# Performance work log

Measured on AMD Instinct MI355X. Metric: run time of the kernel, lower is better.

The kernel has to match this reference:

```python
import jax, jax.numpy as jnp
import numpy as np


def _gcn_conv(h_in, W, b, src, dst, deg_isqrt, n_nodes):
    # PyG GCNConv: out = D^{-1/2} (A + I) D^{-1/2} (h_in @ W) + b
    # src/dst already include self-loops; deg_isqrt precomputed on self-looped graph.
    h = h_in @ W                                   # [N, hid]
    norm = deg_isqrt[src] * deg_isqrt[dst]         # [E+N]
    msg = h[src] * norm[:, None]                   # gather + scale
    agg = jax.ops.segment_sum(msg, dst, num_segments=n_nodes)  # scatter-add
    return agg + b


def setup_inputs() -> dict:
    key = jax.random.key(0)
    ks = jax.random.split(key, 8)
    N, E, P, IN, HID = 100000, 1600000, 400000, 128, 64
    x = jax.random.normal(ks[0], (N, IN), dtype=jnp.float32)
    edge_index = jax.random.randint(ks[1], (2, E), 0, N, dtype=jnp.int64)
    batch = jax.random.randint(ks[2], (N,), 0, 64, dtype=jnp.int64)
    pairs = jax.random.randint(ks[3], (P, 2), 0, N, dtype=jnp.int64)
    s1 = 1.0 / np.sqrt(IN)
    s2 = 1.0 / np.sqrt(HID)
    W1 = jax.random.normal(ks[4], (IN, HID), dtype=jnp.float32) * s1
    b1 = jnp.zeros((HID,), dtype=jnp.float32)
    W2 = jax.random.normal(ks[5], (HID, HID), dtype=jnp.float32) * s2
    b2 = jnp.zeros((HID,), dtype=jnp.float32)
    Wh = jax.random.normal(ks[6], (2 * HID, 1), dtype=jnp.float32) * s2
    bh = jnp.zeros((1,), dtype=jnp.float32)
    return {"x": x, "edge_index": edge_index, "batch": batch, "pairs": pairs,
            "W1": W1, "b1": b1, "W2": W2, "b2": b2, "Wh": Wh, "bh": bh}


def reference(x, edge_index, batch, pairs, W1, b1, W2, b2, Wh, bh):
    n_nodes = x.shape[0]
    loops = jnp.arange(n_nodes, dtype=edge_index.dtype)
    src = jnp.concatenate([edge_index[0], loops])
    dst = jnp.concatenate([edge_index[1], loops])
    # degree on self-looped graph (counted at dst, PyG convention)
    deg = jax.ops.segment_sum(jnp.ones_like(dst, dtype=x.dtype), dst,
                              num_segments=n_nodes)
    deg_isqrt = jnp.where(deg > 0, jax.lax.rsqrt(deg), 0.0)

    h = jax.nn.relu(_gcn_conv(x, W1, b1, src, dst, deg_isqrt, n_nodes))
    h = jax.nn.relu(_gcn_conv(h, W2, b2, src, dst, deg_isqrt, n_nodes))

    emb = jnp.concatenate([h[pairs[:, 0]], h[pairs[:, 1]]], axis=-1)  # [P, 2*hid]
    out = (emb @ Wh + bh)[:, 0]                                        # [P]
    return out
```

## Files before the change

### kernel.cpp

```cpp
#include <hip/hip_runtime.h>

#define THREADS 256
#define BNODES 256
#define PACK_SHIFT 20
#define TILE 8192

__device__ __forceinline__ unsigned short f2bf(float f) {
    unsigned u = __float_as_uint(f);
    unsigned r = (u + 0x7fff + ((u >> 16) & 1)) >> 16;
    return (unsigned short)r;
}
__device__ __forceinline__ float bf2f_lo(unsigned v) { return __uint_as_float(v << 16); }
__device__ __forceinline__ float bf2f_hi(unsigned v) { return __uint_as_float(v & 0xffff0000u); }


__global__ __launch_bounds__(256) void count_buckets(const int* __restrict__ dst,
                                                     int* __restrict__ subcnt,
                                                     int NB, int E) {
    __shared__ int h[1024];
    int t = threadIdx.x;
    for (int i = t; i < NB; i += 256) h[i] = 0;
    __syncthreads();
    int e0 = blockIdx.x * TILE;
    int e1 = min(e0 + TILE, E);
    for (int e = e0 + t; e < e1; e += 256)
        atomicAdd(&h[dst[e] >> 8], 1);
    __syncthreads();
    for (int i = t; i < NB; i += 256)
        if (h[i] > 0) atomicAdd(&subcnt[i], h[i]);
}

__global__ void scan_small_kernel(const int* __restrict__ cnt, int* __restrict__ ptr,
                                  int nb, int total) {
    __shared__ int sh[1024];
    int t = threadIdx.x;
    int v = (t < nb) ? cnt[t] : 0;
    sh[t] = v;
    __syncthreads();
    for (int off = 1; off < 1024; off <<= 1) {
        int add = (t >= off) ? sh[t - off] : 0;
        __syncthreads();
        sh[t] += add;
        __syncthreads();
    }
    if (t < nb) ptr[t] = sh[t] - v;
    if (t == 0) ptr[nb] = total;
}

__global__ __launch_bounds__(256) void block_scatter(const int* __restrict__ src,
                                                     const int* __restrict__ dst,
                                                     const int* __restrict__ subptr,
                                                     int* __restrict__ subcur,
                                                     int* __restrict__ ebuf,
                                                     int NB, int E) {
    __shared__ int h[1024];
    __shared__ int bb[1024];
    int t = threadIdx.x;
    for (int i = t; i < NB; i += 256) h[i] = 0;
    __syncthreads();
    int e0 = blockIdx.x * TILE;
    int e1 = min(e0 + TILE, E);
    for (int e = e0 + t; e < e1; e += 256)
        atomicAdd(&h[dst[e] >> 8], 1);
    __syncthreads();
    for (int i = t; i < NB; i += 256) {
        int c = h[i];
        bb[i] = (c > 0) ? (subptr[i] + atomicAdd(&subcur[i], c)) : 0;
        h[i] = 0;
    }
    __syncthreads();
    for (int e = e0 + t; e < e1; e += 256) {
        int d = dst[e];
        int b = d >> 8;
        int pos = bb[b] + atomicAdd(&h[b], 1);
        ebuf[pos] = src[e] | ((d & (BNODES - 1)) << PACK_SHIFT);
    }
}

__global__ __launch_bounds__(256) void bin_fill_kernel(const int* __restrict__ ebuf,
                                                       const int* __restrict__ subptr,
                                                       int* __restrict__ rowptr,
                                                       float* __restrict__ dis,
                                                       int* __restrict__ srcs,
                                                       int NB, int N, int E) {
    __shared__ int cntL[BNODES];
    __shared__ int rb[BNODES];
    int b = blockIdx.x;
    int t = threadIdx.x;
    int base = b * BNODES;
    int s0 = subptr[b], s1 = subptr[b + 1];
    cntL[t] = 0;
    __syncthreads();
    for (int i = s0 + t; i < s1; i += 256)
        atomicAdd(&cntL[((unsigned)ebuf[i]) >> PACK_SHIFT], 1);
    __syncthreads();
    int myc = cntL[t];
    if (base + t < N) dis[base + t] = rsqrtf((float)myc + 1.0f);
    rb[t] = myc;
    __syncthreads();
    #pragma unroll
    for (int off = 1; off < 256; off <<= 1) {
        int add = (t >= off) ? rb[t - off] : 0;
        __syncthreads();
        rb[t] += add;
        __syncthreads();
    }
    int excl = rb[t] - myc;
    rb[t] = s0 + excl;
    if (base + t < N) rowptr[base + t] = s0 + excl;
    if (b == NB - 1 && t == 0) rowptr[N] = E;
    cntL[t] = 0;
    __syncthreads();
    const int mask = (1 << PACK_SHIFT) - 1;
    for (int i = s0 + t; i < s1; i += 256) {
        int w = ebuf[i];
        int local = ((unsigned)w) >> PACK_SHIFT;
        int pos = rb[local] + atomicAdd(&cntL[local], 1);
        srcs[pos] = w & mask;
    }
}

template<int K, bool SCALE, typename YT>
__global__ __launch_bounds__(256, 4) void gemm_tiled(const float* __restrict__ X,
                                                     const float* __restrict__ W,
                                                     const float* __restrict__ dis,
                                                     YT* __restrict__ Y, int M) {
    __shared__ float Ws[32 * 64];
    __shared__ float Xs[32 * 68];
    const int t = threadIdx.x;

    const int r0 = blockIdx.x * 64;
    const int wave = t >> 6;
    const int lane = t & 63;
    const int tr = lane & 15;
    const int tc = (lane >> 4) + wave * 4;

    float acc[4][4] = {};

    #pragma unroll 1
    for (int kc = 0; kc < K; kc += 32) {
        __syncthreads();
        #pragma unroll
        for (int it = 0; it < 2; ++it) {
            int i = it * 256 + t;
            ((float4*)Ws)[i] = ((const float4*)(W + (size_t)kc * 64))[i];
        }
        #pragma unroll
        for (int it = 0; it < 2; ++it) {
            int i = it * 256 + t;
            int row = i & 63;
            int kq = i >> 6;
            int gr = r0 + row;
            if (gr >= M) gr = M - 1;
            float4 v = *(const float4*)(X + (size_t)gr * K + kc + kq * 4);
            Xs[(kq * 4 + 0) * 68 + row] = v.x;
            Xs[(kq * 4 + 1) * 68 + row] = v.y;
            Xs[(kq * 4 + 2) * 68 + row] = v.z;
            Xs[(kq * 4 + 3) * 68 + row] = v.w;
        }
        __syncthreads();
        #pragma unroll
        for (int kk = 0; kk < 32; ++kk) {
            float4 xv = *(const float4*)(Xs + kk * 68 + tr * 4);
            float4 wv = *(const float4*)(Ws + kk * 64 + tc * 4);
            acc[0][0] = fmaf(xv.x, wv.x, acc[0][0]);
            acc[0][1] = fmaf(xv.x, wv.y, acc[0][1]);
            acc[0][2] = fmaf(xv.x, wv.z, acc[0][2]);
            acc[0][3] = fmaf(xv.x, wv.w, acc[0][3]);
            acc[1][0] = fmaf(xv.y, wv.x, acc[1][0]);
            acc[1][1] = fmaf(xv.y, wv.y, acc[1][1]);
            acc[1][2] = fmaf(xv.y, wv.z, acc[1][2]);
            acc[1][3] = fmaf(xv.y, wv.w, acc[1][3]);
            acc[2][0] = fmaf(xv.z, wv.x, acc[2][0]);
            acc[2][1] = fmaf(xv.z, wv.y, acc[2][1]);
            acc[2][2] = fmaf(xv.z, wv.z, acc[2][2]);
            acc[2][3] = fmaf(xv.z, wv.w, acc[2][3]);
            acc[3][0] = fmaf(xv.w, wv.x, acc[3][0]);
            acc[3][1] = fmaf(xv.w, wv.y, acc[3][1]);
            acc[3][2] = fmaf(xv.w, wv.z, acc[3][2]);
            acc[3][3] = fmaf(xv.w, wv.w, acc[3][3]);
        }
    }

    #pragma unroll
    for (int i = 0; i < 4; ++i) {
        int row = r0 + tr * 4 + i;
        if (row < M) {
            float s = SCALE ? dis[row] : 1.0f;
            if constexpr (sizeof(YT) == 2) {
                ushort4 st;
                st.x = f2bf(acc[i][0] * s);
                st.y = f2bf(acc[i][1] * s);
                st.z = f2bf(acc[i][2] * s);
                st.w = f2bf(acc[i][3] * s);
                *(ushort4*)((unsigned short*)Y + (size_t)row * 64 + tc * 4) = st;
            } else {
                float4 st = make_float4(acc[i][0] * s, acc[i][1] * s,
                                        acc[i][2] * s, acc[i][3] * s);
                *(float4*)((float*)Y + (size_t)row * 64 + tc * 4) = st;
            }
        }
    }
}

template<bool HEAD>
__global__ __launch_bounds__(256) void pull2_kernel(const unsigned* __restrict__ hpre2,
                                                    const int* __restrict__ rowptr,
                                                    const int* __restrict__ srcs,
                                                    const float* __restrict__ dis,
                                                    const float* __restrict__ b,
                                                    const float* __restrict__ Wh,
                                                    float* __restrict__ out,
                                                    float2* __restrict__ s01, int N) {
    int tid = threadIdx.x;
    int wave = tid >> 6;
    int lane = tid & 63;
    int l = lane & 31;
    int node = blockIdx.x * 8 + wave * 2 + (lane >> 5);
    bool valid = node < N;
    int nc = valid ? node : N - 1;
    int i = rowptr[nc];
    int end = valid ? rowptr[nc + 1] : i;

    unsigned sv = hpre2[(size_t)nc * 32 + l];
    float accx = bf2f_lo(sv), accy = bf2f_hi(sv);

    while (__any(i < end)) {
        #pragma unroll
        for (int k = 0; k < 8; ++k) {
            int idx = i + k;
            bool m = idx < end;
            int s = srcs[m ? idx : 0];
            unsigned v = hpre2[(size_t)s * 32 + l];
            accx += m ? bf2f_lo(v) : 0.f;
            accy += m ? bf2f_hi(v) : 0.f;
        }
        i += 8;
    }

    float d = dis[nc];
    float2 bb = ((const float2*)b)[l];
    float ox = accx * d + bb.x;
    float oy = accy * d + bb.y;
    ox = ox > 0.f ? ox : 0.f;
    oy = oy > 0.f ? oy : 0.f;

    if (HEAD) {
        float2 w0 = ((const float2*)Wh)[l];
        float2 w1 = ((const float2*)(Wh + 64))[l];
        float p0 = ox * w0.x + oy * w0.y;
        float p1 = ox * w1.x + oy * w1.y;
        #pragma unroll
        for (int off = 16; off > 0; off >>= 1) {
            p0 += __shfl_down(p0, off, 32);
            p1 += __shfl_down(p1, off, 32);
        }
        if (valid && l == 0) s01[node] = make_float2(p0, p1);
    } else {
        if (valid) *(float2*)(out + (size_t)node * 64 + 2 * l) = make_float2(ox, oy);
    }
}

__global__ void pair_kernel(const float2* __restrict__ s01, const int* __restrict__ pairs,
                            const float* __restrict__ bh, float* __restrict__ out, int P) {
    int p = blockIdx.x * blockDim.x + threadIdx.x;
    if (p < P) {
        int p0 = pairs[2 * (size_t)p];
        int p1 = pairs[2 * (size_t)p + 1];
        out[p] = s01[p0].x + s01[p1].y + bh[0];
    }
}

__global__ void degf_kernel(const int* __restrict__ dst, float* __restrict__ deg, int E) {
    int e = blockIdx.x * blockDim.x + threadIdx.x;
    if (e < E) atomicAdd(&deg[dst[e]], 1.0f);
}
__global__ void rsqrtf_kernel(float* deg, int N) {
    int i = blockIdx.x * blockDim.x + threadIdx.x;
    if (i < N) deg[i] = rsqrtf(deg[i] + 1.0f);
}
__global__ void scatter_kernel(const float* __restrict__ h, const int* __restrict__ src,
                               const int* __restrict__ dst, const float* __restrict__ dis,
                               float* __restrict__ agg, int E, int N) {
    long long idx = (long long)blockIdx.x * blockDim.x + threadIdx.x;
    int e = (int)(idx >> 6);
    int f = (int)(idx & 63);
    if (e >= E + N) return;
    int s, d;
    if (e < E) { s = src[e]; d = dst[e]; } else { s = e - E; d = s; }
    float norm = dis[s] * dis[d];
    atomicAdd(&agg[(size_t)d * 64 + f], h[(size_t)s * 64 + f] * norm);
}
__global__ void bias_relu_kernel(float* __restrict__ buf, const float* __restrict__ b,
                                 long long total) {
    long long i = (long long)blockIdx.x * blockDim.x + threadIdx.x;
    if (i < total) {
        float v = buf[i] + b[(int)(i & 63)];
        buf[i] = v > 0.f ? v : 0.f;
    }
}
__global__ void head_kernel(const float* __restrict__ h, const int* __restrict__ pairs,
                            const float* __restrict__ Wh, const float* __restrict__ bh,
                            float* __restrict__ out, int P) {
    long long idx = (long long)blockIdx.x * blockDim.x + threadIdx.x;
    int p = (int)(idx >> 6);
    int lane = threadIdx.x & 63;
    if (p >= P) return;
    int p0 = pairs[2 * (size_t)p];
    int p1 = pairs[2 * (size_t)p + 1];
    float v = h[(size_t)p0 * 64 + lane] * Wh[lane]
            + h[(size_t)p1 * 64 + lane] * Wh[64 + lane];
    #pragma unroll
    for (int off = 32; off > 0; off >>= 1) v += __shfl_down(v, off);
    if (lane == 0) out[p] = v + bh[0];
}

extern "C" void kernel_launch(void* const* d_in, const int* in_sizes, int n_in,
                              void* d_out, int out_size, void* d_ws, size_t ws_size,
                              hipStream_t stream) {
    const float* x     = (const float*)d_in[0];
    const int*   ei    = (const int*)d_in[1];
    const int*   pairs = (const int*)d_in[3];
    const float* W1    = (const float*)d_in[4];
    const float* b1    = (const float*)d_in[5];
    const float* W2    = (const float*)d_in[6];
    const float* b2    = (const float*)d_in[7];
    const float* Wh    = (const float*)d_in[8];
    const float* bh    = (const float*)d_in[9];

    const int N = in_sizes[0] / 128;
    const int E = in_sizes[1] / 2;
    const int P = in_sizes[3] / 2;
    const int* srcArr = ei;
    const int* dstArr = ei + E;

    const size_t feat_total = (size_t)N * 64;
    const int NB = (N + BNODES - 1) / BNODES;
    const int tileBlocks = (E + TILE - 1) / TILE;
    const int gemm_blocks = (N + 63) / 64;
    const int pull_blocks = (N + 7) / 8;

    auto align512 = [](size_t v) { return (v + 511) & ~(size_t)511; };

    char* ws = (char*)d_ws;
    size_t off = 0;
    float*  dis    = (float*) (ws + off); off += align512((size_t)N * 4);
    int*    rowptr = (int*)   (ws + off); off += align512(((size_t)N + 1) * 4);
    int*    subcnt = (int*)   (ws + off); off += align512((size_t)NB * 4);
    int*    subcur = (int*)   (ws + off); off += align512((size_t)NB * 4);
    int*    subptr = (int*)   (ws + off); off += align512(((size_t)NB + 1) * 4);
    float2* s01    = (float2*)(ws + off); off += align512((size_t)N * 8);
    int*    srcs   = (int*)   (ws + off); off += align512((size_t)E * 4);
    size_t bufA_bytes = align512((size_t)E * 4 > feat_total * 2 ? (size_t)E * 4
                                                                : feat_total * 2);
    unsigned short* bufA = (unsigned short*)(ws + off); off += bufA_bytes;
    float*  bufB   = (float*) (ws + off); off += align512(feat_total * 4);
    int*    ebuf   = (int*)bufA;
    const bool csr_ok = (off <= ws_size) && (NB <= 1024) && (N <= (1 << PACK_SHIFT));

    if (csr_ok) {
        hipMemsetAsync(subcnt, 0, (size_t)NB * 4, stream);
        hipMemsetAsync(subcur, 0, (size_t)NB * 4, stream);
        count_buckets<<<tileBlocks, 256, 0, stream>>>(dstArr, subcnt, NB, E);
        scan_small_kernel<<<1, 1024, 0, stream>>>(subcnt, subptr, NB, E);
        block_scatter<<<tileBlocks, 256, 0, stream>>>(srcArr, dstArr, subptr, subcur,
                                                      ebuf, NB, E);
        bin_fill_kernel<<<NB, 256, 0, stream>>>(ebuf, subptr, rowptr, dis, srcs, NB, N, E);

        gemm_tiled<128, true, unsigned short><<<gemm_blocks, THREADS, 0, stream>>>(
            x, W1, dis, bufA, N);
        pull2_kernel<false><<<pull_blocks, THREADS, 0, stream>>>(
            (const unsigned*)bufA, rowptr, srcs, dis, b1, nullptr, bufB, nullptr, N);

        gemm_tiled<64, true, unsigned short><<<gemm_blocks, THREADS, 0, stream>>>(
            bufB, W2, dis, bufA, N);
        pull2_kernel<true><<<pull_blocks, THREADS, 0, stream>>>(
            (const unsigned*)bufA, rowptr, srcs, dis, b2, Wh, nullptr, s01, N);

        pair_kernel<<<(P + THREADS - 1) / THREADS, THREADS, 0, stream>>>(
            s01, pairs, bh, (float*)d_out, P);
    } else {
        size_t o2 = 0;
        float* deg  = (float*)(ws + o2); o2 += align512((size_t)N * 4);
        float* bA   = (float*)(ws + o2); o2 += align512(feat_total * 4);
        float* bB   = (float*)(ws + o2);
        const size_t edge_threads = (size_t)(E + N) * 64;
        const int eblocks = (E + THREADS - 1) / THREADS;

        hipMemsetAsync(deg, 0, (size_t)N * 4, stream);
        degf_kernel<<<eblocks, THREADS, 0, stream>>>(dstArr, deg, E);
        rsqrtf_kernel<<<(N + THREADS - 1) / THREADS, THREADS, 0, stream>>>(deg, N);

        gemm_tiled<128, false, float><<<gemm_blocks, THREADS, 0, stream>>>(x, W1, deg, bA, N);
        hipMemsetAsync(bB, 0, feat_total * 4, stream);
        scatter_kernel<<<(unsigned)((edge_threads + THREADS - 1) / THREADS), THREADS, 0, stream>>>(
            bA, srcArr, dstArr, deg, bB, E, N);
        bias_relu_kernel<<<(unsigned)((feat_total + THREADS - 1) / THREADS), THREADS, 0, stream>>>(
            bB, b1, (long long)feat_total);

        gemm_tiled<64, false, float><<<gemm_blocks, THREADS, 0, stream>>>(bB, W2, deg, bA, N);
        hipMemsetAsync(bB, 0, feat_total * 4, stream);
        scatter_kernel<<<(unsigned)((edge_threads + THREADS - 1) / THREADS), THREADS, 0, stream>>>(
            bA, srcArr, dstArr, deg, bB, E, N);
        bias_relu_kernel<<<(unsigned)((feat_total + THREADS - 1) / THREADS), THREADS, 0, stream>>>(
            bB, b2, (long long)feat_total);

        head_kernel<<<(unsigned)(((size_t)P * 64 + THREADS - 1) / THREADS), THREADS, 0, stream>>>(
            bB, pairs, Wh, bh, (float*)d_out, P);
    }
}
```

Measured before the change: 198.8 us.

## Split pull gather across two edge streams, fuse memsets, shrink bucket tile

The pull kernel now has each 32-lane half-wave handle two edges at a time: 16 lanes per edge each load a uint2 (four bf16 features), and the two partial sums are combined with a shuffle. This doubles the number of independent row gathers in flight and widens each load. The two memsets become a single zeroing kernel launch, and the bucket tile size shrinks so the count and scatter passes get more blocks. Extra shuffles and partly idle lanes on the final store are the cost, and smaller tiles add more global atomics on the bucket counters.

```diff
diff --git a/kernel.cpp b/kernel.cpp
--- a/kernel.cpp
+++ b/kernel.cpp
@@ -3,7 +3,7 @@
 #define THREADS 256
 #define BNODES 256
 #define PACK_SHIFT 20
-#define TILE 8192
+#define TILE 2048
 
 __device__ __forceinline__ unsigned short f2bf(float f) {
     unsigned u = __float_as_uint(f);
@@ -13,6 +13,10 @@
 __device__ __forceinline__ float bf2f_lo(unsigned v) { return __uint_as_float(v << 16); }
 __device__ __forceinline__ float bf2f_hi(unsigned v) { return __uint_as_float(v & 0xffff0000u); }
 
+
+__global__ void zero2_kernel(int* __restrict__ a, int* __restrict__ b, int n) {
+    for (int i = threadIdx.x; i < n; i += 1024) { a[i] = 0; b[i] = 0; }
+}
 
 __global__ __launch_bounds__(256) void count_buckets(const int* __restrict__ dst,
                                                      int* __restrict__ subcnt,
@@ -213,51 +217,69 @@
                                                     float* __restrict__ out,
                                                     float2* __restrict__ s01, int N) {
     int tid = threadIdx.x;
-    int wave = tid >> 6;
     int lane = tid & 63;
-    int l = lane & 31;
-    int node = blockIdx.x * 8 + wave * 2 + (lane >> 5);
+    int half = lane >> 5;
+    int sub = lane & 31;
+    int eo = sub >> 4;
+    int l = sub & 15;
+    int node = blockIdx.x * 8 + (tid >> 6) * 2 + half;
     bool valid = node < N;
     int nc = valid ? node : N - 1;
-    int i = rowptr[nc];
-    int end = valid ? rowptr[nc + 1] : i;
-
-    unsigned sv = hpre2[(size_t)nc * 32 + l];
-    float accx = bf2f_lo(sv), accy = bf2f_hi(sv);
-
+    int i0 = rowptr[nc];
+    int end = valid ? rowptr[nc + 1] : i0;
+
+    uint2 sv = *(const uint2*)(hpre2 + (size_t)nc * 32 + 2 * l);
+    float a0 = eo ? 0.f : bf2f_lo(sv.x);
+    float a1 = eo ? 0.f : bf2f_hi(sv.x);
+    float a2 = eo ? 0.f : bf2f_lo(sv.y);
+    float a3 = eo ? 0.f : bf2f_hi(sv.y);
+
+    int i = i0 + eo;
     while (__any(i < end)) {
         #pragma unroll
-        for (int k = 0; k < 8; ++k) {
-            int idx = i + k;
+        for (int k = 0; k < 4; ++k) {
+            int idx = i + 2 * k;
             bool m = idx < end;
             int s = srcs[m ? idx : 0];
-            unsigned v = hpre2[(size_t)s * 32 + l];
-            accx += m ? bf2f_lo(v) : 0.f;
-            accy += m ? bf2f_hi(v) : 0.f;
+            uint2 v = *(const uint2*)(hpre2 + (size_t)s * 32 + 2 * l);
+            a0 += m ? bf2f_lo(v.x) : 0.f;
+            a1 += m ? bf2f_hi(v.x) : 0.f;
+            a2 += m ? bf2f_lo(v.y) : 0.f;
+            a3 += m ? bf2f_hi(v.y) : 0.f;
         }
         i += 8;
     }
 
+    a0 += __shfl_down(a0, 16, 32);
+    a1 += __shfl_down(a1, 16, 32);
+    a2 += __shfl_down(a2, 16, 32);
+    a3 += __shfl_down(a3, 16, 32);
+
     float d = dis[nc];
-    float2 bb = ((const float2*)b)[l];
-    float ox = accx * d + bb.x;
-    float oy = accy * d + bb.y;
-    ox = ox > 0.f ? ox : 0.f;
-    oy = oy > 0.f ? oy : 0.f;
+    float4 bb = ((const float4*)b)[l];
+    float o0 = fmaf(a0, d, bb.x);
+    float o1 = fmaf(a1, d, bb.y);
+    float o2 = fmaf(a2, d, bb.z);
+    float o3 = fmaf(a3, d, bb.w);
+    o0 = o0 > 0.f ? o0 : 0.f;
+    o1 = o1 > 0.f ? o1 : 0.f;
+    o2 = o2 > 0.f ? o2 : 0.f;
+    o3 = o3 > 0.f ? o3 : 0.f;
 
     if (HEAD) {
-        float2 w0 = ((const float2*)Wh)[l];
-        float2 w1 = ((const float2*)(Wh + 64))[l];
-        float p0 = ox * w0.x + oy * w0.y;
-        float p1 = ox * w1.x + oy * w1.y;
+        float4 w0 = ((const float4*)Wh)[l];
+        float4 w1 = ((const float4*)(Wh + 64))[l];
+        float p0 = o0 * w0.x + o1 * w0.y + o2 * w0.z + o3 * w0.w;
+        float p1 = o0 * w1.x + o1 * w1.y + o2 * w1.z + o3 * w1.w;
         #pragma unroll
-        for (int off = 16; off > 0; off >>= 1) {
-            p0 += __shfl_down(p0, off, 32);
-            p1 += __shfl_down(p1, off, 32);
-        }
-        if (valid && l == 0) s01[node] = make_float2(p0, p1);
+        for (int off = 8; off > 0; off >>= 1) {
+            p0 += __shfl_down(p0, off, 16);
+            p1 += __shfl_down(p1, off, 16);
+        }
+        if (valid && sub == 0) s01[node] = make_float2(p0, p1);
     } else {
-        if (valid) *(float2*)(out + (size_t)node * 64 + 2 * l) = make_float2(ox, oy);
+        if (valid && eo == 0)
+            *(float4*)(out + (size_t)node * 64 + 4 * l) = make_float4(o0, o1, o2, o3);
     }
 }
 
@@ -359,8 +381,7 @@
     const bool csr_ok = (off <= ws_size) && (NB <= 1024) && (N <= (1 << PACK_SHIFT));
 
     if (csr_ok) {
-        hipMemsetAsync(subcnt, 0, (size_t)NB * 4, stream);
-        hipMemsetAsync(subcur, 0, (size_t)NB * 4, stream);
+        zero2_kernel<<<1, 1024, 0, stream>>>(subcnt, subcur, NB);
         count_buckets<<<tileBlocks, 256, 0, stream>>>(dstArr, subcnt, NB, E);
         scan_small_kernel<<<1, 1024, 0, stream>>>(subcnt, subptr, NB, E);
         block_scatter<<<tileBlocks, 256, 0, stream>>>(srcArr, dstArr, subptr, subcur,
```

New measurement: 200.4 us. Within noise of the previous version (+0.8%).
